# Performance work log

Hardware: AMD Instinct MI355X
Metric: run time of the kernel (lower is better)

Reference implementation:

```python
import jax, jax.numpy as jnp
import numpy as np

N, D, W, S = 16384, 256, 64, 8  # utterances, embed dim, attention half-window, speakers


def setup_inputs() -> dict:
    key = jax.random.key(0)
    ks = jax.random.split(key, 8)
    scale = 1.0 / np.sqrt(D)
    return {
        "x": jax.random.normal(ks[0], (N, D), jnp.float32),
        "speaker_ids": jax.random.randint(ks[1], (N,), 0, S, jnp.int32),
        "W_att": jax.random.normal(ks[2], (D, D), jnp.float32) * scale,
        "W_pred": jax.random.normal(ks[3], (D, D), jnp.float32) * scale,
        "W_suc": jax.random.normal(ks[4], (D, D), jnp.float32) * scale,
        "W_same": jax.random.normal(ks[5], (D, D), jnp.float32) * scale,
        "W_diff": jax.random.normal(ks[6], (D, D), jnp.float32) * scale,
    }


def reference(x, speaker_ids, W_att, W_pred, W_suc, W_same, W_diff):
    n = x.shape[0]
    pad = jnp.zeros((W, D), x.dtype)
    # windowed gather: for utterance i, neighbors at offsets [-W, W-1] (2W slots)
    win_idx = jnp.arange(n)[:, None] + jnp.arange(2 * W)[None, :]  # index into padded [N+2W]
    xp = jnp.concatenate([pad, x, pad], axis=0)                    # [N+2W, D]
    windows = xp[win_idx]                                          # [N, 2W, D]
    # raw_attn[i,w] = (edge_att_weights(windows[i,w])) . x[i]
    raw_attn = jnp.einsum("nwd,ed,ne->nw", windows, W_att, x)      # [N, 2W]
    attn = jax.nn.softmax(raw_attn, axis=1)
    # relation masks over the band: j = i + offset
    offs = jnp.arange(2 * W) - W                                   # [-W, W-1]
    j = jnp.arange(n)[:, None] + offs[None, :]                     # [N, 2W]
    valid = (j >= 0) & (j < n)
    jc = jnp.clip(j, 0, n - 1)
    same_spk = speaker_ids[jc] == speaker_ids[:, None]
    masks = [
        valid & (offs >= 0)[None, :],   # pred: edges to current/future within window
        valid & (offs < 0)[None, :],    # suc: edges to past within window
        valid & same_spk,               # same speaker within window
        valid & ~same_spk,              # different speaker within window
    ]
    # relation-specific GCN aggregation: h = sum_r A_r @ (x @ W_r), A_r banded
    h = jnp.zeros_like(x)
    for Wr, m in zip([W_pred, W_suc, W_same, W_diff], masks):
        support = x @ Wr                                           # [N, D]
        sp = jnp.concatenate([pad, support, pad], axis=0)[win_idx]  # [N, 2W, D]
        h = h + jnp.einsum("nw,nwd->nd", attn * m, sp)
    return jax.nn.log_softmax(h, axis=1)
```

## Files before the change

### kernel.cpp

```cpp
#include <hip/hip_runtime.h>
#include <hip/hip_bf16.h>

typedef unsigned short u16;
typedef unsigned int u32;
typedef __attribute__((ext_vector_type(8))) short short8;
typedef __attribute__((ext_vector_type(4))) float floatx4;

#define NU 16384
#define DIM 256
#define AMS 208
#define ACS 200
#define ACM 12800

#define XHo 0u
#define XLo 4194304u
#define XRo 8388608u
#define YHo 12582912u
#define YLo 16777216u
#define ST0 20971520u
#define STROW 16512u
#define STMAT 4227072u
#define WH0o 33652736u
#define WL0o 33718272u
#define WRo  33783808u

__device__ __forceinline__ u16 bfh(float v) {
  return (u16)(__float_as_uint(v) >> 16);
}
__device__ __forceinline__ float bup(u16 u) {
  return __uint_as_float(((u32)u) << 16);
}
__device__ __forceinline__ u16 bfrn(float v) {
  u32 u = __float_as_uint(v);
  return (u16)((u + 0x7fffu + ((u >> 16) & 1u)) >> 16);
}

__device__ __forceinline__ void gload16(const u16* g, u16* l) {
  __builtin_amdgcn_global_load_lds(
      (__attribute__((address_space(1))) void*)(uintptr_t)g,
      (__attribute__((address_space(3))) void*)(uintptr_t)l, 16, 0, 0);
}

__global__ __launch_bounds__(256) void xprep(const float* __restrict__ x,
                                             u16* __restrict__ ws) {
  int idx = (blockIdx.x * 256 + threadIdx.x) * 8;
  float4 v0 = *(const float4*)(x + idx);
  float4 v1 = *(const float4*)(x + idx + 4);
  float a[8] = {v0.x, v0.y, v0.z, v0.w, v1.x, v1.y, v1.z, v1.w};
  u16 h[8], l[8], r[8];
#pragma unroll
  for (int q = 0; q < 8; ++q) {
    h[q] = bfh(a[q]);
    l[q] = bfh(a[q] - bup(h[q]));
    r[q] = bfrn(a[q]);
  }
  *(uint4*)(ws + XHo + idx) = *(const uint4*)h;
  *(uint4*)(ws + XLo + idx) = *(const uint4*)l;
  *(uint4*)(ws + XRo + idx) = *(const uint4*)r;
}

__global__ __launch_bounds__(256) void wpgz(
    const float* __restrict__ wat, const float* __restrict__ wpr,
    const float* __restrict__ wsu, const float* __restrict__ wsm,
    const float* __restrict__ wdf, u16* __restrict__ ws) {
  const int b = blockIdx.x, t = threadIdx.x;
  if (b < 32) {
    const int s = b & 7, mat = b >> 3, n = t;
    const float* Wa = (mat == 0) ? wat : (mat == 1) ? wpr : (mat == 2) ? wsm : wsu;
    const float* Wb = (mat == 0) ? wat : (mat == 1) ? wsu : (mat == 2) ? wdf : wdf;
    const float c1  = (mat == 0) ? 0.f : (mat == 3) ? 1.f : -1.f;
    u16 hbuf[32], lbuf[32];
#pragma unroll 8
    for (int k = 0; k < 32; ++k) {
      float v = Wa[(s * 32 + k) * 256 + n] + c1 * Wb[(s * 32 + k) * 256 + n];
      if (mat == 0) { hbuf[k] = bfh(v); lbuf[k] = bfh(v - bup(hbuf[k])); }
      else          { hbuf[k] = bfrn(v); }
    }
    u16* dh = ws + ((mat == 0) ? WH0o : (WRo + (size_t)(mat - 1) * 65536))
               + (size_t)s * 8192 + n * 32;
#pragma unroll
    for (int p = 0; p < 4; ++p) *(uint4*)(dh + p * 8) = ((const uint4*)hbuf)[p];
    if (mat == 0) {
      u16* dl = ws + WL0o + (size_t)s * 8192 + n * 32;
#pragma unroll
      for (int p = 0; p < 4; ++p) *(uint4*)(dl + p * 8) = ((const uint4*)lbuf)[p];
    }
  } else {
    int g = (b - 32) * 256 + t;
    int r = g >> 13, rem = g & 8191;
    int d = rem >> 5, p = rem & 31;
    size_t base = ST0 + (size_t)r * STMAT + (size_t)d * STROW;
    size_t off = (p < 16) ? (base + p * 4) : (base + 16448 + (p - 16) * 4);
    *(ushort4*)(ws + off) = make_ushort4(0, 0, 0, 0);
  }
}

__global__ __launch_bounds__(512) void gemmS(u16* __restrict__ ws) {
  __shared__ __align__(16) u16 U[37888];

  const int t = threadIdx.x, path = blockIdx.y, row0 = blockIdx.x * 64;
  const int w = t >> 6, ln = t & 15, quad = (t & 63) >> 4, q8 = quad * 8;
  const int n0 = w * 32;

  if (path == 0) {
#pragma unroll
    for (int cc = 0; cc < 8; ++cc) {
      int idx = t + 512 * cc;
      int buf = idx >> 11, e = idx & 2047;
      int row = e >> 5, c8 = (e & 31) * 8;
      *(uint4*)(U + buf * 16896 + row * 264 + c8) =
          *(const uint4*)(ws + (buf ? XLo : XHo) + (size_t)(row0 + row) * 256 + c8);
    }
    __syncthreads();

    floatx4 acc[4][2];
#pragma unroll
    for (int m = 0; m < 4; ++m)
#pragma unroll
      for (int nt = 0; nt < 2; ++nt) acc[m][nt] = (floatx4){0.f, 0.f, 0.f, 0.f};

    for (int s = 0; s < 8; ++s) {
      short8 ah[4], al[4];
#pragma unroll
      for (int m = 0; m < 4; ++m) {
        ah[m] = *(const short8*)(U + (m * 16 + ln) * 264 + s * 32 + q8);
        al[m] = *(const short8*)(U + 16896 + (m * 16 + ln) * 264 + s * 32 + q8);
      }
      short8 bh[2], bl[2];
#pragma unroll
      for (int nt = 0; nt < 2; ++nt) {
        size_t off = (size_t)s * 8192 + (n0 + nt * 16 + ln) * 32 + q8;
        bh[nt] = *(const short8*)(ws + WH0o + off);
        bl[nt] = *(const short8*)(ws + WL0o + off);
      }
#pragma unroll
      for (int m = 0; m < 4; ++m)
#pragma unroll
        for (int nt = 0; nt < 2; ++nt) {
          acc[m][nt] = __builtin_amdgcn_mfma_f32_16x16x32_bf16(ah[m], bh[nt], acc[m][nt], 0, 0, 0);
          acc[m][nt] = __builtin_amdgcn_mfma_f32_16x16x32_bf16(ah[m], bl[nt], acc[m][nt], 0, 0, 0);
          acc[m][nt] = __builtin_amdgcn_mfma_f32_16x16x32_bf16(al[m], bh[nt], acc[m][nt], 0, 0, 0);
        }
    }
#pragma unroll
    for (int m = 0; m < 4; ++m)
#pragma unroll
      for (int nt = 0; nt < 2; ++nt) {
        int col = n0 + nt * 16 + ln;
#pragma unroll
        for (int r = 0; r < 4; ++r) {
          int row = row0 + m * 16 + quad * 4 + r;
          float y = acc[m][nt][r];
          u16 hh = bfh(y);
          ws[YHo + (size_t)row * 256 + col] = hh;
          ws[YLo + (size_t)row * 256 + col] = bfh(y - bup(hh));
        }
      }
  } else {
#pragma unroll
    for (int cc = 0; cc < 4; ++cc) {
      int idx = t + 512 * cc;
      int row = idx >> 5, c8 = (idx & 31) * 8;
      *(uint4*)(U + row * 264 + c8) =
          *(const uint4*)(ws + XRo + (size_t)(row0 + row) * 256 + c8);
    }
    __syncthreads();

    for (int mat = 0; mat < 3; ++mat) {
      floatx4 acc[4][2];
#pragma unroll
      for (int m = 0; m < 4; ++m)
#pragma unroll
        for (int nt = 0; nt < 2; ++nt) acc[m][nt] = (floatx4){0.f, 0.f, 0.f, 0.f};
      for (int s = 0; s < 8; ++s) {
        short8 ah[4];
#pragma unroll
        for (int m = 0; m < 4; ++m)
          ah[m] = *(const short8*)(U + (m * 16 + ln) * 264 + s * 32 + q8);
        short8 bh[2];
#pragma unroll
        for (int nt = 0; nt < 2; ++nt)
          bh[nt] = *(const short8*)(ws + WRo + (size_t)mat * 65536
                                    + (size_t)s * 8192 + (n0 + nt * 16 + ln) * 32 + q8);
#pragma unroll
        for (int m = 0; m < 4; ++m)
#pragma unroll
          for (int nt = 0; nt < 2; ++nt)
            acc[m][nt] = __builtin_amdgcn_mfma_f32_16x16x32_bf16(ah[m], bh[nt], acc[m][nt], 0, 0, 0);
      }
      __syncthreads();
#pragma unroll
      for (int m = 0; m < 4; ++m)
#pragma unroll
        for (int nt = 0; nt < 2; ++nt) {
          int col = n0 + nt * 16 + ln;
          ushort4 pk = make_ushort4(bfrn(acc[m][nt][0]), bfrn(acc[m][nt][1]),
                                    bfrn(acc[m][nt][2]), bfrn(acc[m][nt][3]));
          *(ushort4*)(U + 16896 + col * 80 + m * 16 + quad * 4) = pk;
        }
      __syncthreads();
      u16* STm = ws + ST0 + (size_t)mat * STMAT;
#pragma unroll
      for (int cc = 0; cc < 4; ++cc) {
        int c = t + 512 * cc;
        int d = c >> 3, part = c & 7;
        *(uint4*)(STm + (size_t)d * STROW + 64 + row0 + part * 8) =
            *(const uint4*)(U + 16896 + d * 80 + part * 8);
      }
    }
  }
}

__global__ __launch_bounds__(512) void fused_attn(
    const u16* __restrict__ ws, const int* __restrict__ spk,
    float* __restrict__ out)
{
  __shared__ __align__(16) u16 big[38400];
  __shared__ __align__(16) u16 Am[64 * AMS];
  __shared__ int spkw[192];
  __shared__ float prt[64][2], prs[64][2];
  __shared__ float red[64][8];

  const int t    = threadIdx.x;
  const int w    = t >> 6;
  const int ln   = t & 15;
  const int quad = (t & 63) >> 4;
  const int q8   = quad * 8;
  const int bswz = (blockIdx.x & 7) * 32 + (blockIdx.x >> 3);
  const int i0   = bswz * 64;
  const int mw   = w & 3;
  const int half = w >> 2;

  if (t < 192) spkw[t] = spk[min(max(i0 - 64 + t, 0), NU - 1)];

  auto STAGE = [&](int ks, int par) {
    const int kd = ks * 32;
    u16* db = big + par * 12288;
#pragma unroll
    for (int cc = 0; cc < 3; ++cc) {
      int idx  = t + 512 * cc;
      int bsel = (idx >= 768) ? 1 : 0;
      int e    = idx - bsel * 768;
      int row  = e >> 2, s = e & 3;
      int sw   = s ^ ((row >> 1) & 3);
      int jc   = min(max(i0 + row - 64, 0), NU - 1);
      const u16* src = ws + (bsel ? XLo : XHo) + (size_t)jc * 256 + kd + sw * 8;
      u16* dst = db + bsel * 6144 + e * 8;
      gload16(src, dst);
    }
  };

  short8 yhv[8], ylv[8];
  {
    const size_t yb = (size_t)(i0 + mw * 16 + ln) * 256 + q8;
#pragma unroll
    for (int ks = 0; ks < 8; ++ks) {
      yhv[ks] = *(const short8*)(ws + YHo + yb + ks * 32);
      ylv[ks] = *(const short8*)(ws + YLo + yb + ks * 32);
    }
  }

  floatx4 accP[6];
#pragma unroll
  for (int cc = 0; cc < 6; ++cc) accP[cc] = (floatx4){0.f, 0.f, 0.f, 0.f};

  STAGE(0, 0);
  __syncthreads();
#pragma unroll
  for (int ks = 0; ks < 8; ++ks) {
    if (ks < 7) STAGE(ks + 1, (ks + 1) & 1);
    const u16* sp = big + (ks & 1) * 12288;
#pragma unroll
    for (int cc = 0; cc < 6; ++cc) {
      int xrow = half * 96 + cc * 16 + ln;
      int slot = quad ^ ((xrow >> 1) & 3);
      const u16* xb = sp + xrow * 32 + slot * 8;
      short8 xbh = *(const short8*)xb;
      short8 xbl = *(const short8*)(xb + 6144);
      accP[cc] = __builtin_amdgcn_mfma_f32_16x16x32_bf16(yhv[ks], xbh, accP[cc], 0, 0, 0);
      accP[cc] = __builtin_amdgcn_mfma_f32_16x16x32_bf16(yhv[ks], xbl, accP[cc], 0, 0, 0);
      accP[cc] = __builtin_amdgcn_mfma_f32_16x16x32_bf16(ylv[ks], xbh, accP[cc], 0, 0, 0);
    }
    __syncthreads();
  }

  int  c_of[6];
  bool vj[6];
#pragma unroll
  for (int cc = 0; cc < 6; ++cc) {
    c_of[cc] = half * 96 + cc * 16 + ln;
    int j = i0 + c_of[cc] - 64;
    vj[cc] = (j >= 0) && (j < NU);
  }
#pragma unroll
  for (int r = 0; r < 4; ++r) {
    int row = mw * 16 + quad * 4 + r;
    float mx = -3.4e38f;
#pragma unroll
    for (int cc = 0; cc < 6; ++cc) {
      int rel = c_of[cc] - row;
      bool inb = (rel >= 0) && (rel < 128);
      if (inb) mx = fmaxf(mx, vj[cc] ? accP[cc][r] : 0.f);
    }
#pragma unroll
    for (int o = 1; o < 16; o <<= 1) mx = fmaxf(mx, __shfl_xor(mx, o));
    if (ln == 0) prt[row][half] = mx;
  }
  __syncthreads();
#pragma unroll
  for (int r = 0; r < 4; ++r) {
    int row = mw * 16 + quad * 4 + r;
    float gm = fmaxf(prt[row][0], prt[row][1]);
    float s = 0.f;
#pragma unroll
    for (int cc = 0; cc < 6; ++cc) {
      int rel = c_of[cc] - row;
      bool inb = (rel >= 0) && (rel < 128);
      float vv = vj[cc] ? accP[cc][r] : 0.f;
      float e  = inb ? __expf(vv - gm) : 0.f;
      s += e;
      accP[cc][r] = (inb && vj[cc]) ? e : 0.f;
    }
#pragma unroll
    for (int o = 1; o < 16; o <<= 1) s += __shfl_xor(s, o);
    if (ln == 0) prs[row][half] = s;
  }
  __syncthreads();
#pragma unroll
  for (int r = 0; r < 4; ++r) {
    int row = mw * 16 + quad * 4 + r;
    float inv = 1.f / (prs[row][0] + prs[row][1]);
#pragma unroll
    for (int cc = 0; cc < 6; ++cc)
      Am[row * AMS + c_of[cc]] = bfrn(accP[cc][r] * inv);
  }
  __syncthreads();

  {
    const int arow = t >> 3, aseg = t & 7;
    const int sr = spkw[arow + 64];
#pragma unroll
    for (int c6 = 0; c6 < 6; ++c6) {
      int cb = c6 * 32 + aseg * 4;
      ushort4 av = *(const ushort4*)(Am + arow * AMS + cb);
      u16 aq[4] = {av.x, av.y, av.z, av.w};
      u16 b0[4], b1[4], b2[4];
#pragma unroll
      for (int q = 0; q < 4; ++q) {
        int c = cb + q;
        b0[q] = (c - arow >= 64) ? aq[q] : (u16)0;
        b1[q] = (spkw[c] == sr) ? aq[q] : (u16)0;
        b2[q] = aq[q];
      }
      *(ushort4*)(big + 0 * ACM + arow * ACS + cb) = *(const ushort4*)b0;
      *(ushort4*)(big + 1 * ACM + arow * ACS + cb) = *(const ushort4*)b1;
      *(ushort4*)(big + 2 * ACM + arow * ACS + cb) = *(const ushort4*)b2;
    }
  }
  __syncthreads();

  const int n0 = w * 32;
  floatx4 acc2[4][2];
#pragma unroll
  for (int m = 0; m < 4; ++m)
#pragma unroll
    for (int nt = 0; nt < 2; ++nt) acc2[m][nt] = (floatx4){0.f, 0.f, 0.f, 0.f};

  for (int kj = 0; kj < 192; kj += 32) {
#pragma unroll
    for (int rel = 0; rel < 3; ++rel) {
      short8 af[4];
#pragma unroll
      for (int m = 0; m < 4; ++m)
        af[m] = *(const short8*)(big + rel * ACM + (m * 16 + ln) * ACS + kj + q8);
#pragma unroll
      for (int nt = 0; nt < 2; ++nt) {
        size_t so = (size_t)ST0 + (size_t)rel * STMAT
                  + (size_t)(n0 + nt * 16 + ln) * STROW + (size_t)(i0 + kj) + q8;
        short8 bf8 = *(const short8*)(ws + so);
#pragma unroll
        for (int m = 0; m < 4; ++m)
          acc2[m][nt] = __builtin_amdgcn_mfma_f32_16x16x32_bf16(af[m], bf8, acc2[m][nt], 0, 0, 0);
      }
    }
  }

#pragma unroll
  for (int m = 0; m < 4; ++m)
#pragma unroll
    for (int r = 0; r < 4; ++r) {
      float v = fmaxf(acc2[m][0][r], acc2[m][1][r]);
#pragma unroll
      for (int o = 1; o < 16; o <<= 1) v = fmaxf(v, __shfl_xor(v, o));
      if (ln == 0) red[m * 16 + quad * 4 + r][w] = v;
    }
  __syncthreads();
  float gmx[4][4];
#pragma unroll
  for (int m = 0; m < 4; ++m)
#pragma unroll
    for (int r = 0; r < 4; ++r) {
      int row = m * 16 + quad * 4 + r;
      float g = red[row][0];
#pragma unroll
      for (int ww = 1; ww < 8; ++ww) g = fmaxf(g, red[row][ww]);
      gmx[m][r] = g;
    }
  __syncthreads();
#pragma unroll
  for (int m = 0; m < 4; ++m)
#pragma unroll
    for (int r = 0; r < 4; ++r) {
      float e = __expf(acc2[m][0][r] - gmx[m][r]) + __expf(acc2[m][1][r] - gmx[m][r]);
#pragma unroll
      for (int o = 1; o < 16; o <<= 1) e += __shfl_xor(e, o);
      if (ln == 0) red[m * 16 + quad * 4 + r][w] = e;
    }
  __syncthreads();
#pragma unroll
  for (int m = 0; m < 4; ++m)
#pragma unroll
    for (int r = 0; r < 4; ++r) {
      int row = m * 16 + quad * 4 + r;
      float s = red[row][0];
#pragma unroll
      for (int ww = 1; ww < 8; ++ww) s += red[row][ww];
      float lse = gmx[m][r] + logf(s);
      size_t rowg = (size_t)(i0 + row) * DIM;
      out[rowg + n0 + ln]      = acc2[m][0][r] - lse;
      out[rowg + n0 + 16 + ln] = acc2[m][1][r] - lse;
    }
}

extern "C" void kernel_launch(void* const* d_in, const int* in_sizes, int n_in,
                              void* d_out, int out_size, void* d_ws, size_t ws_size,
                              hipStream_t stream) {
  const float* x   = (const float*)d_in[0];
  const int*   spk = (const int*)d_in[1];
  const float* wat = (const float*)d_in[2];
  const float* wpr = (const float*)d_in[3];
  const float* wsu = (const float*)d_in[4];
  const float* wsm = (const float*)d_in[5];
  const float* wdf = (const float*)d_in[6];
  float* out = (float*)d_out;
  u16* ws = (u16*)d_ws;

  hipLaunchKernelGGL(xprep, dim3(2048), dim3(256), 0, stream, x, ws);
  hipLaunchKernelGGL(wpgz, dim3(128), dim3(256), 0, stream,
                     wat, wpr, wsu, wsm, wdf, ws);
  hipLaunchKernelGGL(gemmS, dim3(256, 2), dim3(512), 0, stream, ws);
  hipLaunchKernelGGL(fused_attn, dim3(256), dim3(512), 0, stream, ws, spk, out);
}
```

Measured before the change: 147.4 us.

## Fuse Y=x·W_att GEMM into attention kernel, merge prep kernels, retile support GEMM

Merges the x-split and weight-prep kernels into one launch. The x·W_att split-bf16 GEMM moves into fused_attn, so each block computes its own 64-row Y tile in shared memory and the YH/YL global round trip goes away. The support GEMM becomes a separate kernel with 32-row tiles that computes all three relation matrices in one pass and uses 512 blocks. The cost is a larger shared-memory footprint in fused_attn, which may lower occupancy and delays its start.

After: 146.9 us. Within noise of the previous version (-0.3%).

```diff
diff --git a/kernel.cpp b/kernel.cpp
--- a/kernel.cpp
+++ b/kernel.cpp
@@ -12,11 +12,13 @@
 #define ACS 200
 #define ACM 12800
 
+#define YLO 16896u
+#define STGo 33792u
+#define AMB 58368u
+
 #define XHo 0u
 #define XLo 4194304u
 #define XRo 8388608u
-#define YHo 12582912u
-#define YLo 16777216u
 #define ST0 20971520u
 #define STROW 16512u
 #define STMAT 4227072u
@@ -41,31 +43,32 @@
       (__attribute__((address_space(3))) void*)(uintptr_t)l, 16, 0, 0);
 }
 
-__global__ __launch_bounds__(256) void xprep(const float* __restrict__ x,
-                                             u16* __restrict__ ws) {
-  int idx = (blockIdx.x * 256 + threadIdx.x) * 8;
-  float4 v0 = *(const float4*)(x + idx);
-  float4 v1 = *(const float4*)(x + idx + 4);
-  float a[8] = {v0.x, v0.y, v0.z, v0.w, v1.x, v1.y, v1.z, v1.w};
-  u16 h[8], l[8], r[8];
-#pragma unroll
-  for (int q = 0; q < 8; ++q) {
-    h[q] = bfh(a[q]);
-    l[q] = bfh(a[q] - bup(h[q]));
-    r[q] = bfrn(a[q]);
-  }
-  *(uint4*)(ws + XHo + idx) = *(const uint4*)h;
-  *(uint4*)(ws + XLo + idx) = *(const uint4*)l;
-  *(uint4*)(ws + XRo + idx) = *(const uint4*)r;
-}
-
-__global__ __launch_bounds__(256) void wpgz(
+__global__ __launch_bounds__(256) void prep(
+    const float* __restrict__ x,
     const float* __restrict__ wat, const float* __restrict__ wpr,
     const float* __restrict__ wsu, const float* __restrict__ wsm,
     const float* __restrict__ wdf, u16* __restrict__ ws) {
   const int b = blockIdx.x, t = threadIdx.x;
-  if (b < 32) {
-    const int s = b & 7, mat = b >> 3, n = t;
+  if (b < 2048) {
+    int idx = (b * 256 + t) * 8;
+    float4 v0 = *(const float4*)(x + idx);
+    float4 v1 = *(const float4*)(x + idx + 4);
+    float a[8] = {v0.x, v0.y, v0.z, v0.w, v1.x, v1.y, v1.z, v1.w};
+    u16 h[8], l[8], r[8];
+#pragma unroll
+    for (int q = 0; q < 8; ++q) {
+      h[q] = bfh(a[q]);
+      l[q] = bfh(a[q] - bup(h[q]));
+      r[q] = bfrn(a[q]);
+    }
+    *(uint4*)(ws + XHo + idx) = *(const uint4*)h;
+    *(uint4*)(ws + XLo + idx) = *(const uint4*)l;
+    *(uint4*)(ws + XRo + idx) = *(const uint4*)r;
+    return;
+  }
+  const int b2 = b - 2048;
+  if (b2 < 32) {
+    const int s = b2 & 7, mat = b2 >> 3, n = t;
     const float* Wa = (mat == 0) ? wat : (mat == 1) ? wpr : (mat == 2) ? wsm : wsu;
     const float* Wb = (mat == 0) ? wat : (mat == 1) ? wsu : (mat == 2) ? wdf : wdf;
     const float c1  = (mat == 0) ? 0.f : (mat == 3) ? 1.f : -1.f;
@@ -86,7 +89,7 @@
       for (int p = 0; p < 4; ++p) *(uint4*)(dl + p * 8) = ((const uint4*)lbuf)[p];
     }
   } else {
-    int g = (b - 32) * 256 + t;
+    int g = (b2 - 32) * 256 + t;
     int r = g >> 13, rem = g & 8191;
     int d = rem >> 5, p = rem & 31;
     size_t base = ST0 + (size_t)r * STMAT + (size_t)d * STROW;
@@ -95,128 +98,79 @@
   }
 }
 
-__global__ __launch_bounds__(512) void gemmS(u16* __restrict__ ws) {
-  __shared__ __align__(16) u16 U[37888];
-
-  const int t = threadIdx.x, path = blockIdx.y, row0 = blockIdx.x * 64;
+__global__ __launch_bounds__(512, 4) void gemmS1(u16* __restrict__ ws) {
+  __shared__ __align__(16) u16 U[39168];
+
+  const int t = threadIdx.x, row0 = blockIdx.x * 32;
   const int w = t >> 6, ln = t & 15, quad = (t & 63) >> 4, q8 = quad * 8;
   const int n0 = w * 32;
 
-  if (path == 0) {
-#pragma unroll
-    for (int cc = 0; cc < 8; ++cc) {
-      int idx = t + 512 * cc;
-      int buf = idx >> 11, e = idx & 2047;
-      int row = e >> 5, c8 = (e & 31) * 8;
-      *(uint4*)(U + buf * 16896 + row * 264 + c8) =
-          *(const uint4*)(ws + (buf ? XLo : XHo) + (size_t)(row0 + row) * 256 + c8);
-    }
-    __syncthreads();
-
-    floatx4 acc[4][2];
-#pragma unroll
-    for (int m = 0; m < 4; ++m)
-#pragma unroll
-      for (int nt = 0; nt < 2; ++nt) acc[m][nt] = (floatx4){0.f, 0.f, 0.f, 0.f};
-
-    for (int s = 0; s < 8; ++s) {
-      short8 ah[4], al[4];
-#pragma unroll
-      for (int m = 0; m < 4; ++m) {
-        ah[m] = *(const short8*)(U + (m * 16 + ln) * 264 + s * 32 + q8);
-        al[m] = *(const short8*)(U + 16896 + (m * 16 + ln) * 264 + s * 32 + q8);
-      }
-      short8 bh[2], bl[2];
-#pragma unroll
-      for (int nt = 0; nt < 2; ++nt) {
-        size_t off = (size_t)s * 8192 + (n0 + nt * 16 + ln) * 32 + q8;
-        bh[nt] = *(const short8*)(ws + WH0o + off);
-        bl[nt] = *(const short8*)(ws + WL0o + off);
-      }
-#pragma unroll
-      for (int m = 0; m < 4; ++m)
-#pragma unroll
-        for (int nt = 0; nt < 2; ++nt) {
-          acc[m][nt] = __builtin_amdgcn_mfma_f32_16x16x32_bf16(ah[m], bh[nt], acc[m][nt], 0, 0, 0);
-          acc[m][nt] = __builtin_amdgcn_mfma_f32_16x16x32_bf16(ah[m], bl[nt], acc[m][nt], 0, 0, 0);
-          acc[m][nt] = __builtin_amdgcn_mfma_f32_16x16x32_bf16(al[m], bh[nt], acc[m][nt], 0, 0, 0);
-        }
-    }
-#pragma unroll
-    for (int m = 0; m < 4; ++m)
+#pragma unroll
+  for (int cc = 0; cc < 2; ++cc) {
+    int idx = t + 512 * cc;
+    int row = idx >> 5, c8 = (idx & 31) * 8;
+    *(uint4*)(U + row * 264 + c8) =
+        *(const uint4*)(ws + XRo + (size_t)(row0 + row) * 256 + c8);
+  }
+  __syncthreads();
+
+  floatx4 acc[3][2][2];
+#pragma unroll
+  for (int mat = 0; mat < 3; ++mat)
+#pragma unroll
+    for (int m = 0; m < 2; ++m)
+#pragma unroll
+      for (int nt = 0; nt < 2; ++nt) acc[mat][m][nt] = (floatx4){0.f, 0.f, 0.f, 0.f};
+
+  for (int s = 0; s < 8; ++s) {
+    short8 ah[2];
+#pragma unroll
+    for (int m = 0; m < 2; ++m)
+      ah[m] = *(const short8*)(U + (m * 16 + ln) * 264 + s * 32 + q8);
+#pragma unroll
+    for (int mat = 0; mat < 3; ++mat) {
+      short8 bh[2];
+#pragma unroll
+      for (int nt = 0; nt < 2; ++nt)
+        bh[nt] = *(const short8*)(ws + WRo + (size_t)mat * 65536
+                                  + (size_t)s * 8192 + (n0 + nt * 16 + ln) * 32 + q8);
+#pragma unroll
+      for (int m = 0; m < 2; ++m)
+#pragma unroll
+        for (int nt = 0; nt < 2; ++nt)
+          acc[mat][m][nt] = __builtin_amdgcn_mfma_f32_16x16x32_bf16(ah[m], bh[nt], acc[mat][m][nt], 0, 0, 0);
+    }
+  }
+
+#pragma unroll
+  for (int mat = 0; mat < 3; ++mat)
+#pragma unroll
+    for (int m = 0; m < 2; ++m)
 #pragma unroll
       for (int nt = 0; nt < 2; ++nt) {
         int col = n0 + nt * 16 + ln;
-#pragma unroll
-        for (int r = 0; r < 4; ++r) {
-          int row = row0 + m * 16 + quad * 4 + r;
-          float y = acc[m][nt][r];
-          u16 hh = bfh(y);
-          ws[YHo + (size_t)row * 256 + col] = hh;
-          ws[YLo + (size_t)row * 256 + col] = bfh(y - bup(hh));
-        }
-      }
-  } else {
-#pragma unroll
-    for (int cc = 0; cc < 4; ++cc) {
-      int idx = t + 512 * cc;
-      int row = idx >> 5, c8 = (idx & 31) * 8;
-      *(uint4*)(U + row * 264 + c8) =
-          *(const uint4*)(ws + XRo + (size_t)(row0 + row) * 256 + c8);
-    }
-    __syncthreads();
-
-    for (int mat = 0; mat < 3; ++mat) {
-      floatx4 acc[4][2];
-#pragma unroll
-      for (int m = 0; m < 4; ++m)
-#pragma unroll
-        for (int nt = 0; nt < 2; ++nt) acc[m][nt] = (floatx4){0.f, 0.f, 0.f, 0.f};
-      for (int s = 0; s < 8; ++s) {
-        short8 ah[4];
-#pragma unroll
-        for (int m = 0; m < 4; ++m)
-          ah[m] = *(const short8*)(U + (m * 16 + ln) * 264 + s * 32 + q8);
-        short8 bh[2];
-#pragma unroll
-        for (int nt = 0; nt < 2; ++nt)
-          bh[nt] = *(const short8*)(ws + WRo + (size_t)mat * 65536
-                                    + (size_t)s * 8192 + (n0 + nt * 16 + ln) * 32 + q8);
-#pragma unroll
-        for (int m = 0; m < 4; ++m)
-#pragma unroll
-          for (int nt = 0; nt < 2; ++nt)
-            acc[m][nt] = __builtin_amdgcn_mfma_f32_16x16x32_bf16(ah[m], bh[nt], acc[m][nt], 0, 0, 0);
-      }
-      __syncthreads();
-#pragma unroll
-      for (int m = 0; m < 4; ++m)
-#pragma unroll
-        for (int nt = 0; nt < 2; ++nt) {
-          int col = n0 + nt * 16 + ln;
-          ushort4 pk = make_ushort4(bfrn(acc[m][nt][0]), bfrn(acc[m][nt][1]),
-                                    bfrn(acc[m][nt][2]), bfrn(acc[m][nt][3]));
-          *(ushort4*)(U + 16896 + col * 80 + m * 16 + quad * 4) = pk;
-        }
-      __syncthreads();
-      u16* STm = ws + ST0 + (size_t)mat * STMAT;
-#pragma unroll
-      for (int cc = 0; cc < 4; ++cc) {
-        int c = t + 512 * cc;
-        int d = c >> 3, part = c & 7;
-        *(uint4*)(STm + (size_t)d * STROW + 64 + row0 + part * 8) =
-            *(const uint4*)(U + 16896 + d * 80 + part * 8);
-      }
-    }
-  }
+        ushort4 pk = make_ushort4(bfrn(acc[mat][m][nt][0]), bfrn(acc[mat][m][nt][1]),
+                                  bfrn(acc[mat][m][nt][2]), bfrn(acc[mat][m][nt][3]));
+        *(ushort4*)(U + 8448 + mat * 10240 + col * 40 + m * 16 + quad * 4) = pk;
+      }
+  __syncthreads();
+
+#pragma unroll
+  for (int mat = 0; mat < 3; ++mat)
+#pragma unroll
+    for (int cc = 0; cc < 2; ++cc) {
+      int c = t + 512 * cc;
+      int d = c >> 2, part = c & 3;
+      *(uint4*)(ws + ST0 + (size_t)mat * STMAT + (size_t)d * STROW + 64 + row0 + part * 8) =
+          *(const uint4*)(U + 8448 + mat * 10240 + d * 40 + part * 8);
+    }
 }
 
 __global__ __launch_bounds__(512) void fused_attn(
     const u16* __restrict__ ws, const int* __restrict__ spk,
     float* __restrict__ out)
 {
-  __shared__ __align__(16) u16 big[38400];
-  __shared__ __align__(16) u16 Am[64 * AMS];
+  __shared__ __align__(16) u16 U[71680];
   __shared__ int spkw[192];
   __shared__ float prt[64][2], prs[64][2];
   __shared__ float red[64][8];
@@ -230,12 +184,71 @@
   const int i0   = bswz * 64;
   const int mw   = w & 3;
   const int half = w >> 2;
+  const int n0   = w * 32;
 
   if (t < 192) spkw[t] = spk[min(max(i0 - 64 + t, 0), NU - 1)];
+
+  {
+#pragma unroll
+    for (int cc = 0; cc < 8; ++cc) {
+      int idx = t + 512 * cc;
+      int buf = idx >> 11, e = idx & 2047;
+      int row = e >> 5, c8 = (e & 31) * 8;
+      *(uint4*)(U + buf * YLO + row * 264 + c8) =
+          *(const uint4*)(ws + (buf ? XLo : XHo) + (size_t)(i0 + row) * 256 + c8);
+    }
+    __syncthreads();
+
+    floatx4 acc[4][2];
+#pragma unroll
+    for (int m = 0; m < 4; ++m)
+#pragma unroll
+      for (int nt = 0; nt < 2; ++nt) acc[m][nt] = (floatx4){0.f, 0.f, 0.f, 0.f};
+
+    for (int s = 0; s < 8; ++s) {
+      short8 ah[4], al[4];
+#pragma unroll
+      for (int m = 0; m < 4; ++m) {
+        ah[m] = *(const short8*)(U + (m * 16 + ln) * 264 + s * 32 + q8);
+        al[m] = *(const short8*)(U + YLO + (m * 16 + ln) * 264 + s * 32 + q8);
+      }
+      short8 bh[2], bl[2];
+#pragma unroll
+      for (int nt = 0; nt < 2; ++nt) {
+        size_t off = (size_t)s * 8192 + (n0 + nt * 16 + ln) * 32 + q8;
+        bh[nt] = *(const short8*)(ws + WH0o + off);
+        bl[nt] = *(const short8*)(ws + WL0o + off);
+      }
+#pragma unroll
+      for (int m = 0; m < 4; ++m)
+#pragma unroll
+        for (int nt = 0; nt < 2; ++nt) {
+          acc[m][nt] = __builtin_amdgcn_mfma_f32_16x16x32_bf16(ah[m], bh[nt], acc[m][nt], 0, 0, 0);
+          acc[m][nt] = __builtin_amdgcn_mfma_f32_16x16x32_bf16(ah[m], bl[nt], acc[m][nt], 0, 0, 0);
+          acc[m][nt] = __builtin_amdgcn_mfma_f32_16x16x32_bf16(al[m], bh[nt], acc[m][nt], 0, 0, 0);
+        }
+    }
+    __syncthreads();
+
+#pragma unroll
+    for (int m = 0; m < 4; ++m)
+#pragma unroll
+      for (int nt = 0; nt < 2; ++nt) {
+        int col = n0 + nt * 16 + ln;
+#pragma unroll
+        for (int r = 0; r < 4; ++r) {
+          int row = m * 16 + quad * 4 + r;
+          float y = acc[m][nt][r];
+          u16 hh = bfh(y);
+          U[row * 264 + col] = hh;
+          U[YLO + row * 264 + col] = bfh(y - bup(hh));
+        }
+      }
+  }
 
   auto STAGE = [&](int ks, int par) {
     const int kd = ks * 32;
-    u16* db = big + par * 12288;
+    u16* db = U + STGo + par * 12288;
 #pragma unroll
     for (int cc = 0; cc < 3; ++cc) {
       int idx  = t + 512 * cc;
@@ -250,16 +263,6 @@
     }
   };
 
-  short8 yhv[8], ylv[8];
-  {
-    const size_t yb = (size_t)(i0 + mw * 16 + ln) * 256 + q8;
-#pragma unroll
-    for (int ks = 0; ks < 8; ++ks) {
-      yhv[ks] = *(const short8*)(ws + YHo + yb + ks * 32);
-      ylv[ks] = *(const short8*)(ws + YLo + yb + ks * 32);
-    }
-  }
-
   floatx4 accP[6];
 #pragma unroll
   for (int cc = 0; cc < 6; ++cc) accP[cc] = (floatx4){0.f, 0.f, 0.f, 0.f};
@@ -269,7 +272,10 @@
 #pragma unroll
   for (int ks = 0; ks < 8; ++ks) {
     if (ks < 7) STAGE(ks + 1, (ks + 1) & 1);
-    const u16* sp = big + (ks & 1) * 12288;
+    const u16* sp = U + STGo + (ks & 1) * 12288;
+    const u16* yb = U + (mw * 16 + ln) * 264 + ks * 32 + q8;
+    short8 yh8 = *(const short8*)yb;
+    short8 yl8 = *(const short8*)(yb + YLO);
 #pragma unroll
     for (int cc = 0; cc < 6; ++cc) {
       int xrow = half * 96 + cc * 16 + ln;
@@ -277,9 +283,9 @@
       const u16* xb = sp + xrow * 32 + slot * 8;
       short8 xbh = *(const short8*)xb;
       short8 xbl = *(const short8*)(xb + 6144);
-      accP[cc] = __builtin_amdgcn_mfma_f32_16x16x32_bf16(yhv[ks], xbh, accP[cc], 0, 0, 0);
-      accP[cc] = __builtin_amdgcn_mfma_f32_16x16x32_bf16(yhv[ks], xbl, accP[cc], 0, 0, 0);
-      accP[cc] = __builtin_amdgcn_mfma_f32_16x16x32_bf16(ylv[ks], xbh, accP[cc], 0, 0, 0);
+      accP[cc] = __builtin_amdgcn_mfma_f32_16x16x32_bf16(yh8, xbh, accP[cc], 0, 0, 0);
+      accP[cc] = __builtin_amdgcn_mfma_f32_16x16x32_bf16(yh8, xbl, accP[cc], 0, 0, 0);
+      accP[cc] = __builtin_amdgcn_mfma_f32_16x16x32_bf16(yl8, xbh, accP[cc], 0, 0, 0);
     }
     __syncthreads();
   }
@@ -332,7 +338,7 @@
     float inv = 1.f / (prs[row][0] + prs[row][1]);
 #pragma unroll
     for (int cc = 0; cc < 6; ++cc)
-      Am[row * AMS + c_of[cc]] = bfrn(accP[cc][r] * inv);
+      U[AMB + row * AMS + c_of[cc]] = bfrn(accP[cc][r] * inv);
   }
   __syncthreads();
 
@@ -342,7 +348,7 @@
 #pragma unroll
     for (int c6 = 0; c6 < 6; ++c6) {
       int cb = c6 * 32 + aseg * 4;
-      ushort4 av = *(const ushort4*)(Am + arow * AMS + cb);
+      ushort4 av = *(const ushort4*)(U + AMB + arow * AMS + cb);
       u16 aq[4] = {av.x, av.y, av.z, av.w};
       u16 b0[4], b1[4], b2[4];
 #pragma unroll
@@ -352,14 +358,13 @@
         b1[q] = (spkw[c] == sr) ? aq[q] : (u16)0;
         b2[q] = aq[q];
       }
-      *(ushort4*)(big + 0 * ACM + arow * ACS + cb) = *(const ushort4*)b0;
-      *(ushort4*)(big + 1 * ACM + arow * ACS + cb) = *(const ushort4*)b1;
-      *(ushort4*)(big + 2 * ACM + arow * ACS + cb) = *(const ushort4*)b2;
-    }
-  }
-  __syncthreads();
-
-  const int n0 = w * 32;
+      *(ushort4*)(U + 0 * ACM + arow * ACS + cb) = *(const ushort4*)b0;
+      *(ushort4*)(U + 1 * ACM + arow * ACS + cb) = *(const ushort4*)b1;
+      *(ushort4*)(U + 2 * ACM + arow * ACS + cb) = *(const ushort4*)b2;
+    }
+  }
+  __syncthreads();
+
   floatx4 acc2[4][2];
 #pragma unroll
   for (int m = 0; m < 4; ++m)
@@ -372,7 +377,7 @@
       short8 af[4];
 #pragma unroll
       for (int m = 0; m < 4; ++m)
-        af[m] = *(const short8*)(big + rel * ACM + (m * 16 + ln) * ACS + kj + q8);
+        af[m] = *(const short8*)(U + rel * ACM + (m * 16 + ln) * ACS + kj + q8);
 #pragma unroll
       for (int nt = 0; nt < 2; ++nt) {
         size_t so = (size_t)ST0 + (size_t)rel * STMAT
@@ -445,9 +450,8 @@
   float* out = (float*)d_out;
   u16* ws = (u16*)d_ws;
 
-  hipLaunchKernelGGL(xprep, dim3(2048), dim3(256), 0, stream, x, ws);
-  hipLaunchKernelGGL(wpgz, dim3(128), dim3(256), 0, stream,
-                     wat, wpr, wsu, wsm, wdf, ws);
-  hipLaunchKernelGGL(gemmS, dim3(256, 2), dim3(512), 0, stream, ws);
+  hipLaunchKernelGGL(prep, dim3(2176), dim3(256), 0, stream,
+                     x, wat, wpr, wsu, wsm, wdf, ws);
+  hipLaunchKernelGGL(gemmS1, dim3(512), dim3(512), 0, stream, ws);
   hipLaunchKernelGGL(fused_attn, dim3(256), dim3(512), 0, stream, ws, spk, out);
 }
```
